# Performance work log

Measured on AMD Instinct MI355X. Metric: run time of the kernel, lower is better.

Reference implementation:

```python
import jax, jax.numpy as jnp
import numpy as np

B, L, DM = 4, 2048, 1024  # batch, seq len (== l_max, global kernel), d_model; head_dim = 1


def setup_inputs() -> dict:
    key = jax.random.key(0)
    ks = jax.random.split(key, 13)
    n = lambda k, shape, s=1.0: jax.random.normal(k, shape, dtype=jnp.float32) * s
    W_SCALE = 0.02   # keeps activations well-conditioned through the chained convs
    K_SCALE = 0.02
    return {
        "u": n(ks[0], (B, L, DM)),
        "Wq": n(ks[1], (DM, DM), W_SCALE), "bq": n(ks[2], (DM,), W_SCALE),
        "Wk": n(ks[3], (DM, DM), W_SCALE), "bk": n(ks[4], (DM,), W_SCALE),
        "Wv": n(ks[5], (DM, DM), W_SCALE), "bv": n(ks[6], (DM,), W_SCALE),
        "k_kernel": n(ks[7], (DM, L), K_SCALE),
        "k_D": n(ks[8], (DM,)),
        "ssm_kernel": n(ks[9], (DM, L), K_SCALE),
        "D": n(ks[10], (DM,)),
        "Wo": n(ks[11], (DM, DM), W_SCALE), "bo": n(ks[12], (DM,), W_SCALE),
    }


def reference(u, Wq, bq, Wk, bk, Wv, bv, k_kernel, k_D, ssm_kernel, D, Wo, bo):
    # u: (B, L, H) with H = d_model (head_dim = 1)
    Lseq = u.shape[1]
    fft_size = 2 * Lseq  # zero-pad to 2L for linear (causal) convolution

    # q/k/v projections -> (B, H, L)
    q = jnp.einsum('blh,dh->bdl', u, Wq) + bq[None, :, None]
    k = jnp.einsum('blh,dh->bdl', u, Wk) + bk[None, :, None]
    v = jnp.einsum('blh,dh->bdl', u, Wv) + bv[None, :, None]

    # shift conv on k: k <- k_kernel * k (causal FFT conv) + k_D * k
    k_kernel_f = jnp.fft.rfft(k_kernel, n=fft_size)           # (H, F)
    k_f = jnp.fft.rfft(k, n=fft_size)                          # (B, H, F)
    shift_k = jnp.fft.irfft(k_kernel_f[None] * k_f, n=fft_size)[..., :Lseq]
    k = shift_k + k_D[None, :, None] * k

    # head_dim == 1: kv outer product collapses to elementwise gate
    kv = k * v                                                 # (B, H, L)

    # ssm conv on kv (torch's 1/fft_size + norm='forward' irfft == standard irfft)
    kv_f = jnp.fft.rfft(kv, n=fft_size)                        # (B, H, F)
    ssm_kernel_f = jnp.fft.rfft(ssm_kernel, n=fft_size)        # (H, F)
    y = jnp.fft.irfft(kv_f * ssm_kernel_f[None], n=fft_size)[..., :Lseq]
    y = y + kv * D[None, :, None]                              # D skip

    # q gating, then output projection
    y = y * q                                                  # (B, H, L)
    y = jnp.swapaxes(y, 1, 2)                                  # (B, L, H)
    return jnp.einsum('blh,oh->blo', y, Wo) + bo
```

## Files before the change

### kernel.cpp

```cpp
#include <hip/hip_runtime.h>
#include <hip/hip_bf16.h>
#include <stdint.h>

#define DM   1024
#define LSEQ 2048
#define NB   4

typedef __attribute__((ext_vector_type(8))) short  short8;
typedef __attribute__((ext_vector_type(4))) float  floatx4;

__device__ __forceinline__ ushort f2b(float x) {
    union { float f; uint32_t u; } v; v.f = x;
    uint32_t b = v.u + 0x7FFF + ((v.u >> 16) & 1);
    return (ushort)(b >> 16);
}
__device__ __forceinline__ float b2f(ushort x) {
    union { uint32_t u; float f; } v; v.u = ((uint32_t)x) << 16;
    return v.f;
}

__global__ __launch_bounds__(256) void cvt_bf16_kernel(const float* __restrict__ in,
                                                       ushort* __restrict__ out, int n8) {
    int i = blockIdx.x * 256 + threadIdx.x;
    if (i >= n8) return;
    const float4* p = (const float4*)in + (size_t)i * 2;
    float4 a = p[0], b = p[1];
    union { ushort us[8]; uint4 v; } o;
    o.us[0] = f2b(a.x); o.us[1] = f2b(a.y); o.us[2] = f2b(a.z); o.us[3] = f2b(a.w);
    o.us[4] = f2b(b.x); o.us[5] = f2b(b.y); o.us[6] = f2b(b.z); o.us[7] = f2b(b.w);
    ((uint4*)out)[i] = o.v;
}

__global__ __launch_bounds__(256) void cvt_w_kernel(const float* __restrict__ Wq,
                                                    const float* __restrict__ Wk,
                                                    const float* __restrict__ Wv,
                                                    const float* __restrict__ Wo,
                                                    ushort* __restrict__ dst) {
    const int per = DM * DM / 8;
    int i = blockIdx.x * 256 + threadIdx.x;
    int r = i / per;
    const float* src = (r == 0) ? Wq : (r == 1) ? Wk : (r == 2) ? Wv : Wo;
    int j = i - r * per;
    const float4* p = (const float4*)src + (size_t)j * 2;
    float4 a = p[0], b = p[1];
    union { ushort us[8]; uint4 v; } o;
    o.us[0] = f2b(a.x); o.us[1] = f2b(a.y); o.us[2] = f2b(a.z); o.us[3] = f2b(a.w);
    o.us[4] = f2b(b.x); o.us[5] = f2b(b.y); o.us[6] = f2b(b.z); o.us[7] = f2b(b.w);
    ((uint4*)dst)[i] = o.v;
}

template <int MODE>
__global__ __launch_bounds__(512, 2) void gemm_8p(const ushort* __restrict__ Aw,
                                                  const ushort* __restrict__ Bw,
                                                  const float* __restrict__ b0,
                                                  const float* __restrict__ b1,
                                                  const float* __restrict__ b2,
                                                  void* __restrict__ C0v,
                                                  void* __restrict__ C1v,
                                                  void* __restrict__ C2v,
                                                  int N, int nbx) {
    constexpr int K = 1024, BK = 64, NT = K / BK;
    __shared__ char lds[131072];

    const int tid   = threadIdx.x;
    const int wave  = tid >> 6;
    const int lane  = tid & 63;
    const int qlane = lane & 15;
    const int qk    = lane >> 4;
    const int z7    = qlane & 7;
    const int wm    = wave >> 2;
    const int wn    = wave & 3;

    int flat = blockIdx.y * nbx + blockIdx.x;
    int nwg  = nbx * gridDim.y;
    int swz  = (flat & 7) * (nwg >> 3) + (flat >> 3);
    const int tn = (swz % nbx) * 256;
    const int tm = (swz / nbx) * 256;

    const int srcChunkOff   = (((lane & 7) ^ (lane >> 3)) * 8);
    const int srcRowInSlice = (lane >> 3);

#define STAGE_H(TT, ISB, H)                                                                   \
    {                                                                                         \
        const ushort* gbase = (ISB) ? Bw : Aw;                                                \
        const int trow = ((ISB) ? tn : tm) + (H) * 128 + wave * 16 + srcRowInSlice;           \
        char* dst = lds + ((ISB) ? 65536 : 0) + ((((TT) & 1) * 2 + (H)) * 16384) + wave * 2048; \
        const int k0_ = (TT) * BK;                                                            \
        _Pragma("unroll")                                                                     \
        for (int j = 0; j < 2; ++j) {                                                         \
            const ushort* src = gbase + (size_t)(trow + j * 8) * K + k0_ + srcChunkOff;       \
            __builtin_amdgcn_global_load_lds(                                                 \
                (const __attribute__((address_space(1))) void*)src,                           \
                (__attribute__((address_space(3))) void*)(dst + j * 1024), 16, 0, 0);         \
        }                                                                                     \
    }

    short8 af[4][2], bf0[2][2], bf1[2][2];
    floatx4 acc[2][2][4][2] = {};

#define LDA(TT, MH)                                                                           \
    {                                                                                         \
        const char* Ab = lds + ((((TT) & 1) * 2 + (MH)) * 16384);                             \
        _Pragma("unroll")                                                                     \
        for (int i = 0; i < 4; ++i) {                                                         \
            int lr = wm * 64 + i * 16 + qlane;                                                \
            _Pragma("unroll")                                                                 \
            for (int ks = 0; ks < 2; ++ks)                                                    \
                af[i][ks] = *(const short8*)(Ab + lr * 128 + (((ks * 4 + qk) ^ z7) << 4));    \
        }                                                                                     \
    }
#define LDB(TT, NH, BF)                                                                       \
    {                                                                                         \
        const char* Bb = lds + 65536 + ((((TT) & 1) * 2 + (NH)) * 16384);                     \
        _Pragma("unroll")                                                                     \
        for (int j = 0; j < 2; ++j) {                                                         \
            int lr = wn * 32 + j * 16 + qlane;                                                \
            _Pragma("unroll")                                                                 \
            for (int ks = 0; ks < 2; ++ks)                                                    \
                BF[j][ks] = *(const short8*)(Bb + lr * 128 + (((ks * 4 + qk) ^ z7) << 4));    \
        }                                                                                     \
    }
#define MFMAQ(MH, NH, BF)                                                                     \
    __builtin_amdgcn_s_setprio(1);                                                           \
    _Pragma("unroll")                                                                         \
    for (int ks = 0; ks < 2; ++ks)                                                            \
        _Pragma("unroll")                                                                     \
        for (int i = 0; i < 4; ++i)                                                           \
            _Pragma("unroll")                                                                 \
            for (int j = 0; j < 2; ++j)                                                       \
                acc[MH][NH][i][j] = __builtin_amdgcn_mfma_f32_16x16x32_bf16(                  \
                    af[i][ks], BF[j][ks], acc[MH][NH][i][j], 0, 0, 0);                        \
    __builtin_amdgcn_s_setprio(0);
#define BAR  __builtin_amdgcn_s_barrier(); __builtin_amdgcn_sched_barrier(0)
#define LGKM0 asm volatile("s_waitcnt lgkmcnt(0)" ::: "memory"); __builtin_amdgcn_sched_barrier(0)

    STAGE_H(0, 0, 0); STAGE_H(0, 1, 0); STAGE_H(0, 1, 1); STAGE_H(0, 0, 1);
    STAGE_H(1, 0, 0); STAGE_H(1, 1, 0); STAGE_H(1, 1, 1);
    asm volatile("s_waitcnt vmcnt(6)" ::: "memory");
    __builtin_amdgcn_s_barrier();
    __builtin_amdgcn_sched_barrier(0);

    for (int t = 0; t < NT; ++t) {
        LDA(t, 0);
        LDB(t, 0, bf0);
        if (t + 1 < NT) STAGE_H(t + 1, 0, 1);
        BAR; LGKM0;
        MFMAQ(0, 0, bf0);
        BAR;
        LDB(t, 1, bf1);
        if (t + 2 < NT) STAGE_H(t + 2, 0, 0);
        BAR; LGKM0;
        MFMAQ(0, 1, bf1);
        BAR;
        LDA(t, 1);
        if (t + 2 < NT) STAGE_H(t + 2, 1, 0);
        BAR; LGKM0;
        MFMAQ(1, 0, bf0);
        BAR;
        if (t + 2 < NT) STAGE_H(t + 2, 1, 1);
        if (t + 2 < NT)      { asm volatile("s_waitcnt vmcnt(6)" ::: "memory"); }
        else if (t + 1 < NT) { asm volatile("s_waitcnt vmcnt(0)" ::: "memory"); }
        BAR; LGKM0;
        MFMAQ(1, 1, bf1);
        BAR;
    }
#undef STAGE_H
#undef LDA
#undef LDB
#undef MFMAQ
#undef BAR
#undef LGKM0

#pragma unroll
    for (int mh = 0; mh < 2; ++mh)
#pragma unroll
    for (int nh = 0; nh < 2; ++nh)
#pragma unroll
    for (int i = 0; i < 4; ++i)
#pragma unroll
    for (int j = 0; j < 2; ++j) {
        int n  = tn + nh * 128 + wn * 32 + j * 16 + qlane;
        int m0 = tm + mh * 128 + wm * 64 + i * 16 + qk * 4;
        if (MODE == 0) {
            int proj = n >> 10, dd = n & (DM - 1);
            const float* bb = (proj == 0) ? b0 : (proj == 1) ? b1 : b2;
            ushort* Cb      = (ushort*)((proj == 0) ? C0v : (proj == 1) ? C1v : C2v);
            float bv = bb[dd];
            int b = m0 >> 11, l = m0 & (LSEQ - 1);
            ushort4 val;
            val.x = f2b(acc[mh][nh][i][j][0] + bv);
            val.y = f2b(acc[mh][nh][i][j][1] + bv);
            val.z = f2b(acc[mh][nh][i][j][2] + bv);
            val.w = f2b(acc[mh][nh][i][j][3] + bv);
            *(ushort4*)(Cb + ((size_t)b * DM + dd) * LSEQ + l) = val;
        } else {
            float* C0 = (float*)C0v;
            float bv = b0[n];
#pragma unroll
            for (int r = 0; r < 4; ++r)
                C0[(size_t)(m0 + r) * N + n] = acc[mh][nh][i][j][r] + bv;
        }
    }
}

template <int MODE>
__global__ __launch_bounds__(512, 2) void gemm_bt2(const ushort* __restrict__ Aw,
                                                   const ushort* __restrict__ Bw,
                                                   const float* __restrict__ b0,
                                                   const float* __restrict__ b1,
                                                   const float* __restrict__ b2,
                                                   void* __restrict__ C0v,
                                                   void* __restrict__ C1v,
                                                   void* __restrict__ C2v,
                                                   int M, int N, int K, int nbx) {
    constexpr int BM = 128, BN = 256, BK = 64;
    constexpr int BUFB = 49152;
    __shared__ char lds[3 * BUFB];

    const int tid   = threadIdx.x;
    const int wave  = tid >> 6;
    const int lane  = tid & 63;
    const int qlane = lane & 15;
    const int qk    = lane >> 4;

    int flat = blockIdx.y * nbx + blockIdx.x;
    int nwg  = nbx * gridDim.y;
    int swz  = (flat & 7) * (nwg >> 3) + (flat >> 3);
    const int tn = (swz % nbx) * BN;
    const int tm = (swz / nbx) * BM;

    const int wmo = (wave >> 2) * 64;
    const int wno = (wave & 3) * 64;
    const int NT  = K / BK;

#define STAGE(kt, p)                                                                          \
    {                                                                                         \
        const int k0_ = (kt) * BK;                                                            \
        char* Ab_ = lds + (p) * BUFB;                                                         \
        char* Bb_ = Ab_ + 16384;                                                              \
        _Pragma("unroll")                                                                     \
        for (int j = 0; j < 2; ++j) {                                                         \
            int id = wave * 64 + lane + j * 512;                                              \
            int row = id >> 3, s = id & 7;                                                    \
            const ushort* src = Aw + (size_t)(tm + row) * K + k0_ + ((s ^ (row & 7)) * 8);    \
            __builtin_amdgcn_global_load_lds((const __attribute__((address_space(1))) void*)src, \
                (__attribute__((address_space(3))) void*)(Ab_ + wave * 1024 + j * 8192), 16, 0, 0); \
        }                                                                                     \
        _Pragma("unroll")                                                                     \
        for (int j = 0; j < 4; ++j) {                                                         \
            int id = wave * 64 + lane + j * 512;                                              \
            int row = id >> 3, s = id & 7;                                                    \
            const ushort* src = Bw + (size_t)(tn + row) * K + k0_ + ((s ^ (row & 7)) * 8);    \
            __builtin_amdgcn_global_load_lds((const __attribute__((address_space(1))) void*)src, \
                (__attribute__((address_space(3))) void*)(Bb_ + wave * 1024 + j * 8192), 16, 0, 0); \
        }                                                                                     \
    }

    floatx4 acc[4][4] = {};

    STAGE(0, 0);
    STAGE(1, 1);

    const int z7 = qlane & 7;

    for (int t = 0; t < NT; ++t) {
        const int cur = t % 3;
        if (t < NT - 1) asm volatile("s_waitcnt vmcnt(6)" ::: "memory");
        else            asm volatile("s_waitcnt vmcnt(0)" ::: "memory");
        __builtin_amdgcn_s_barrier();
        __builtin_amdgcn_sched_barrier(0);

        if (t + 2 < NT) STAGE(t + 2, (t + 2) % 3);

        const char* Ab = lds + cur * BUFB;
        const char* Bb = Ab + 16384;
#pragma unroll
        for (int kk = 0; kk < 2; ++kk) {
            const int slot = ((kk * 4 + qk) ^ z7) << 4;
            short8 af[4], bfv[4];
#pragma unroll
            for (int i = 0; i < 4; ++i) {
                int r = wmo + i * 16 + qlane;
                af[i] = *(const short8*)(Ab + r * 128 + slot);
            }
#pragma unroll
            for (int j = 0; j < 4; ++j) {
                int r = wno + j * 16 + qlane;
                bfv[j] = *(const short8*)(Bb + r * 128 + slot);
            }
            __builtin_amdgcn_s_setprio(1);
#pragma unroll
            for (int i = 0; i < 4; ++i)
#pragma unroll
                for (int j = 0; j < 4; ++j)
                    acc[i][j] = __builtin_amdgcn_mfma_f32_16x16x32_bf16(af[i], bfv[j], acc[i][j], 0, 0, 0);
            __builtin_amdgcn_s_setprio(0);
        }
    }
#undef STAGE

#pragma unroll
    for (int i = 0; i < 4; ++i) {
#pragma unroll
        for (int j = 0; j < 4; ++j) {
            int n  = tn + wno + j * 16 + qlane;
            int m0 = tm + wmo + i * 16 + qk * 4;
            if (MODE == 0) {
                int proj = n >> 10, dd = n & (DM - 1);
                const float* bb = (proj == 0) ? b0 : (proj == 1) ? b1 : b2;
                ushort* Cb      = (ushort*)((proj == 0) ? C0v : (proj == 1) ? C1v : C2v);
                float bv = bb[dd];
                int b = m0 >> 11, l = m0 & (LSEQ - 1);
                ushort4 val;
                val.x = f2b(acc[i][j][0] + bv);
                val.y = f2b(acc[i][j][1] + bv);
                val.z = f2b(acc[i][j][2] + bv);
                val.w = f2b(acc[i][j][3] + bv);
                *(ushort4*)(Cb + ((size_t)b * DM + dd) * LSEQ + l) = val;
            } else {
                float* C0 = (float*)C0v;
                float bv = b0[n];
#pragma unroll
                for (int r = 0; r < 4; ++r)
                    C0[(size_t)(m0 + r) * N + n] = acc[i][j][r] + bv;
            }
        }
    }
}

#define KSTR 2096
#define XSTR 2248

__global__ __launch_bounds__(512) void conv_mfma_kernel(const ushort* __restrict__ x,
                                                        const float* __restrict__ ker,
                                                        const float* __restrict__ scale,
                                                        const ushort* __restrict__ gate,
                                                        ushort* __restrict__ out) {
    __shared__ ushort krev[KSTR];
    __shared__ ushort xs[4 * XSTR];
    const int d    = blockIdx.x;
    const int tid  = threadIdx.x;
    const int wave = tid >> 6;
    const int lane = tid & 63;

    {
        int b = wave >> 1, half = wave & 1;
        const ushort* src = x + ((size_t)b * DM + d) * LSEQ + half * 1024 + lane * 8;
        char* dst = (char*)xs + b * (XSTR * 2) + 256 + half * 2048;
#pragma unroll
        for (int c = 0; c < 2; ++c)
            __builtin_amdgcn_global_load_lds((const __attribute__((address_space(1))) void*)(src + c * 512),
                                             (__attribute__((address_space(3))) void*)(dst + c * 1024),
                                             16, 0, 0);
    }
    {
        const float* krow = ker + (size_t)d * LSEQ;
        int e0 = tid * 4;
        float4 kv = *(const float4*)(krow + e0);
        ushort4 o;
        o.x = f2b(kv.w); o.y = f2b(kv.z); o.z = f2b(kv.y); o.w = f2b(kv.x);
        *(ushort4*)(krev + (2060 - e0)) = o;
        uint4 z = {0, 0, 0, 0};
        if (tid < 2)  *(uint4*)((char*)krev + tid * 16) = z;
        if (tid >= 2 && tid < 6) *(uint4*)((char*)krev + 4128 + (tid - 2) * 16) = z;
        if (tid >= 64 && tid < 128) {
            int b = (tid - 64) >> 4, c = (tid - 64) & 15;
            *(uint4*)((char*)xs + b * (XSTR * 2) + c * 16) = z;
        }
        if (tid >= 128 && tid < 144) {
            int b = (tid - 128) >> 2, c = (tid - 128) & 3;
            *(uint4*)((char*)xs + b * (XSTR * 2) + 4352 + c * 16) = z;
        }
    }
    __syncthreads();

    const int qn = lane & 15;
    const int qk = lane >> 4;

    int g[2] = {wave, 15 - wave};
    const int smax_all = 128 * (15 - wave) + 128;

    const int lbase = (qn & 3) * XSTR + 128 + 16 * (qn >> 2) + 8 * qk;

    floatx4 acc[2][2] = {};

    short8 fE[2], fO[2];
#pragma unroll
    for (int gi = 0; gi < 2; ++gi) {
        fE[gi] = *(const short8*)(xs + lbase + 128 * g[gi] + 64);
        fO[gi] = *(const short8*)(xs + lbase + 128 * g[gi] + 32);
    }

#define CSTEP(SS, FP)                                                                        \
    {                                                                                        \
        int b_el = 2063 - qn + 8 * qk - (SS);                                                \
        int A0 = b_el & ~3;                                                                  \
        uint2 w0 = *(const uint2*)(krev + A0);                                               \
        uint2 w1 = *(const uint2*)(krev + A0 + 4);                                           \
        uint2 w2 = *(const uint2*)(krev + A0 + 8);                                           \
        int qsel = (b_el >> 1) & 1;                                                          \
        uint sh  = (uint)(b_el & 1) * 16u;                                                   \
        uint e0 = qsel ? w0.y : w0.x;                                                        \
        uint e1 = qsel ? w1.x : w0.y;                                                        \
        uint e2 = qsel ? w1.y : w1.x;                                                        \
        uint e3 = qsel ? w2.x : w1.y;                                                        \
        uint e4 = qsel ? w2.y : w2.x;                                                        \
        union { uint u[4]; short8 v; } Af;                                                   \
        Af.u[0] = __builtin_amdgcn_alignbit(e1, e0, sh);                                     \
        Af.u[1] = __builtin_amdgcn_alignbit(e2, e1, sh);                                     \
        Af.u[2] = __builtin_amdgcn_alignbit(e3, e2, sh);                                     \
        Af.u[3] = __builtin_amdgcn_alignbit(e4, e3, sh);                                     \
        _Pragma("unroll")                                                                    \
        for (int gi = 0; gi < 2; ++gi) {                                                     \
            if ((SS) <= 128 * g[gi] + 128) {                                                 \
                short8 fN = *(const short8*)(xs + lbase + 128 * g[gi] - (SS));               \
                acc[gi][0] = __builtin_amdgcn_mfma_f32_16x16x32_bf16(Af.v, fN, acc[gi][0], 0, 0, 0); \
                acc[gi][1] = __builtin_amdgcn_mfma_f32_16x16x32_bf16(Af.v, FP[gi], acc[gi][1], 0, 0, 0); \
                FP[gi] = fN;                                                                 \
            }                                                                                \
        }                                                                                    \
    }

    for (int s = 0; s <= smax_all; s += 64) {
        CSTEP(s, fE);
        if (s + 32 <= smax_all) CSTEP(s + 32, fO);
    }
#undef CSTEP

    const float sc = scale[d];
#pragma unroll
    for (int gi = 0; gi < 2; ++gi) {
#pragma unroll
        for (int m = 0; m < 2; ++m) {
            int p  = 8 * g[gi] + 4 * m + (qn >> 2);
            int b  = qn & 3;
            int l0 = 16 * p + 4 * qk;
            size_t off = ((size_t)b * DM + d) * LSEQ + l0;
            ushort4 xv = *(const ushort4*)(xs + b * XSTR + 128 + l0);
            ushort4 gv = *(const ushort4*)(gate + off);
            ushort4 ov;
            ov.x = f2b((acc[gi][m][0] + sc * b2f(xv.x)) * b2f(gv.x));
            ov.y = f2b((acc[gi][m][1] + sc * b2f(xv.y)) * b2f(gv.y));
            ov.z = f2b((acc[gi][m][2] + sc * b2f(xv.z)) * b2f(gv.z));
            ov.w = f2b((acc[gi][m][3] + sc * b2f(xv.w)) * b2f(gv.w));
            *(ushort4*)(out + off) = ov;
        }
    }
}

__global__ __launch_bounds__(256) void transpose_bf16(const ushort* __restrict__ in,
                                                      ushort* __restrict__ out) {
    __shared__ ushort t[32][36];
    const int l0 = blockIdx.x * 32;
    const int d0 = blockIdx.y * 32;
    const int b  = blockIdx.z;
    const int q  = threadIdx.x & 7;
    const int r  = threadIdx.x >> 3;
    *(ushort4*)(&t[r][q * 4]) = *(const ushort4*)(in + ((size_t)b * DM + d0 + r) * LSEQ + l0 + q * 4);
    __syncthreads();
    ushort4 o;
    o.x = t[q * 4 + 0][r]; o.y = t[q * 4 + 1][r]; o.z = t[q * 4 + 2][r]; o.w = t[q * 4 + 3][r];
    *(ushort4*)(out + ((size_t)b * LSEQ + l0 + r) * DM + d0 + q * 4) = o;
}

extern "C" void kernel_launch(void* const* d_in, const int* in_sizes, int n_in,
                              void* d_out, int out_size, void* d_ws, size_t ws_size,
                              hipStream_t stream) {
    const float* u        = (const float*)d_in[0];
    const float* Wq       = (const float*)d_in[1];
    const float* bq       = (const float*)d_in[2];
    const float* Wk       = (const float*)d_in[3];
    const float* bk       = (const float*)d_in[4];
    const float* Wv       = (const float*)d_in[5];
    const float* bv       = (const float*)d_in[6];
    const float* k_kernel = (const float*)d_in[7];
    const float* k_D      = (const float*)d_in[8];
    const float* ssm_ker  = (const float*)d_in[9];
    const float* Dv       = (const float*)d_in[10];
    const float* Wo       = (const float*)d_in[11];
    const float* bo       = (const float*)d_in[12];
    float* outp = (float*)d_out;

    char* ws = (char*)d_ws;
    ushort* Q    = (ushort*)(ws);
    ushort* KV   = (ushort*)(ws + (16ull << 20));
    ushort* V    = (ushort*)(ws + (32ull << 20));
    ushort* U16  = (ushort*)(ws + (48ull << 20));
    ushort* YT   = (ushort*)(ws + (64ull << 20));
    ushort* Wcat = (ushort*)(ws + (80ull << 20));

    cvt_bf16_kernel<<<(NB * LSEQ * DM / 8) / 256, 256, 0, stream>>>(u, U16, NB * LSEQ * DM / 8);
    cvt_w_kernel<<<(4 * DM * DM / 8) / 256, 256, 0, stream>>>(Wq, Wk, Wv, Wo, Wcat);

    dim3 g1(3 * DM / 256, NB * LSEQ / 256);
    gemm_8p<0><<<g1, 512, 0, stream>>>(U16, Wcat, bq, bk, bv, Q, KV, V,
                                       3 * DM, 3 * DM / 256);

    conv_mfma_kernel<<<DM, 512, 0, stream>>>(KV, k_kernel, k_D, V, KV);
    conv_mfma_kernel<<<DM, 512, 0, stream>>>(KV, ssm_ker, Dv, Q, KV);

    dim3 g2(LSEQ / 32, DM / 32, NB);
    transpose_bf16<<<g2, 256, 0, stream>>>(KV, YT);

    dim3 g3(DM / 256, NB * LSEQ / 128);
    gemm_bt2<1><<<g3, 512, 0, stream>>>(YT, Wcat + 3 * DM * DM, bo, bo, bo,
                                        outp, outp, outp, NB * LSEQ, DM, DM, DM / 256);
}
```

Measured before the change: 173.2 us.

## Software-pipeline LDS fragment loads across MFMA quadrants and fuse conversion kernels

New measurement: 166.4 us. -4.0%, faster.

```diff
diff --git a/kernel.cpp b/kernel.cpp
--- a/kernel.cpp
+++ b/kernel.cpp
@@ -19,34 +19,31 @@
     return v.f;
 }
 
-__global__ __launch_bounds__(256) void cvt_bf16_kernel(const float* __restrict__ in,
-                                                       ushort* __restrict__ out, int n8) {
-    int i = blockIdx.x * 256 + threadIdx.x;
-    if (i >= n8) return;
-    const float4* p = (const float4*)in + (size_t)i * 2;
-    float4 a = p[0], b = p[1];
-    union { ushort us[8]; uint4 v; } o;
-    o.us[0] = f2b(a.x); o.us[1] = f2b(a.y); o.us[2] = f2b(a.z); o.us[3] = f2b(a.w);
-    o.us[4] = f2b(b.x); o.us[5] = f2b(b.y); o.us[6] = f2b(b.z); o.us[7] = f2b(b.w);
-    ((uint4*)out)[i] = o.v;
-}
-
-__global__ __launch_bounds__(256) void cvt_w_kernel(const float* __restrict__ Wq,
-                                                    const float* __restrict__ Wk,
-                                                    const float* __restrict__ Wv,
-                                                    const float* __restrict__ Wo,
-                                                    ushort* __restrict__ dst) {
+__global__ __launch_bounds__(256) void cvt_all_kernel(const float* __restrict__ u,
+                                                      const float* __restrict__ Wq,
+                                                      const float* __restrict__ Wk,
+                                                      const float* __restrict__ Wv,
+                                                      const float* __restrict__ Wo,
+                                                      ushort* __restrict__ U16,
+                                                      ushort* __restrict__ Wcat) {
+    const int nu  = NB * LSEQ * DM / 8;
     const int per = DM * DM / 8;
     int i = blockIdx.x * 256 + threadIdx.x;
-    int r = i / per;
-    const float* src = (r == 0) ? Wq : (r == 1) ? Wk : (r == 2) ? Wv : Wo;
-    int j = i - r * per;
+    const float* src; ushort* dst; int j;
+    if (i < nu) { src = u; dst = U16; j = i; }
+    else {
+        int k = i - nu;
+        int r = k / per;
+        src = (r == 0) ? Wq : (r == 1) ? Wk : (r == 2) ? Wv : Wo;
+        dst = Wcat + (size_t)r * (DM * DM);
+        j = k - r * per;
+    }
     const float4* p = (const float4*)src + (size_t)j * 2;
     float4 a = p[0], b = p[1];
     union { ushort us[8]; uint4 v; } o;
     o.us[0] = f2b(a.x); o.us[1] = f2b(a.y); o.us[2] = f2b(a.z); o.us[3] = f2b(a.w);
     o.us[4] = f2b(b.x); o.us[5] = f2b(b.y); o.us[6] = f2b(b.z); o.us[7] = f2b(b.w);
-    ((uint4*)dst)[i] = o.v;
+    *(uint4*)(dst + (size_t)j * 8) = o.v;
 }
 
 template <int MODE>
@@ -95,10 +92,10 @@
         }                                                                                     \
     }
 
-    short8 af[4][2], bf0[2][2], bf1[2][2];
+    short8 af[4][2], af2[4][2], bf0[2][2], bf1[2][2];
     floatx4 acc[2][2][4][2] = {};
 
-#define LDA(TT, MH)                                                                           \
+#define LDA(TT, MH, AF)                                                                       \
     {                                                                                         \
         const char* Ab = lds + ((((TT) & 1) * 2 + (MH)) * 16384);                             \
         _Pragma("unroll")                                                                     \
@@ -106,7 +103,7 @@
             int lr = wm * 64 + i * 16 + qlane;                                                \
             _Pragma("unroll")                                                                 \
             for (int ks = 0; ks < 2; ++ks)                                                    \
-                af[i][ks] = *(const short8*)(Ab + lr * 128 + (((ks * 4 + qk) ^ z7) << 4));    \
+                AF[i][ks] = *(const short8*)(Ab + lr * 128 + (((ks * 4 + qk) ^ z7) << 4));    \
         }                                                                                     \
     }
 #define LDB(TT, NH, BF)                                                                       \
@@ -120,7 +117,7 @@
                 BF[j][ks] = *(const short8*)(Bb + lr * 128 + (((ks * 4 + qk) ^ z7) << 4));    \
         }                                                                                     \
     }
-#define MFMAQ(MH, NH, BF)                                                                     \
+#define MFMAQ(MH, NH, AF, BF)                                                                 \
     __builtin_amdgcn_s_setprio(1);                                                           \
     _Pragma("unroll")                                                                         \
     for (int ks = 0; ks < 2; ++ks)                                                            \
@@ -129,47 +126,40 @@
             _Pragma("unroll")                                                                 \
             for (int j = 0; j < 2; ++j)                                                       \
                 acc[MH][NH][i][j] = __builtin_amdgcn_mfma_f32_16x16x32_bf16(                  \
-                    af[i][ks], BF[j][ks], acc[MH][NH][i][j], 0, 0, 0);                        \
+                    AF[i][ks], BF[j][ks], acc[MH][NH][i][j], 0, 0, 0);                        \
     __builtin_amdgcn_s_setprio(0);
-#define BAR  __builtin_amdgcn_s_barrier(); __builtin_amdgcn_sched_barrier(0)
-#define LGKM0 asm volatile("s_waitcnt lgkmcnt(0)" ::: "memory"); __builtin_amdgcn_sched_barrier(0)
+#define BARX  __builtin_amdgcn_s_barrier(); __builtin_amdgcn_sched_barrier(0)
 
     STAGE_H(0, 0, 0); STAGE_H(0, 1, 0); STAGE_H(0, 1, 1); STAGE_H(0, 0, 1);
     STAGE_H(1, 0, 0); STAGE_H(1, 1, 0); STAGE_H(1, 1, 1);
     asm volatile("s_waitcnt vmcnt(6)" ::: "memory");
-    __builtin_amdgcn_s_barrier();
-    __builtin_amdgcn_sched_barrier(0);
+    BARX;
+    LDA(0, 0, af); LDB(0, 0, bf0);
 
     for (int t = 0; t < NT; ++t) {
-        LDA(t, 0);
-        LDB(t, 0, bf0);
         if (t + 1 < NT) STAGE_H(t + 1, 0, 1);
-        BAR; LGKM0;
-        MFMAQ(0, 0, bf0);
-        BAR;
         LDB(t, 1, bf1);
+        MFMAQ(0, 0, af, bf0);
+        BARX;
         if (t + 2 < NT) STAGE_H(t + 2, 0, 0);
-        BAR; LGKM0;
-        MFMAQ(0, 1, bf1);
-        BAR;
-        LDA(t, 1);
+        LDA(t, 1, af2);
+        MFMAQ(0, 1, af, bf1);
+        BARX;
         if (t + 2 < NT) STAGE_H(t + 2, 1, 0);
-        BAR; LGKM0;
-        MFMAQ(1, 0, bf0);
-        BAR;
+        MFMAQ(1, 0, af2, bf0);
+        BARX;
         if (t + 2 < NT) STAGE_H(t + 2, 1, 1);
         if (t + 2 < NT)      { asm volatile("s_waitcnt vmcnt(6)" ::: "memory"); }
         else if (t + 1 < NT) { asm volatile("s_waitcnt vmcnt(0)" ::: "memory"); }
-        BAR; LGKM0;
-        MFMAQ(1, 1, bf1);
-        BAR;
+        BARX;
+        if (t + 1 < NT) { LDA(t + 1, 0, af); LDB(t + 1, 0, bf0); }
+        MFMAQ(1, 1, af2, bf1);
     }
 #undef STAGE_H
 #undef LDA
 #undef LDB
 #undef MFMAQ
-#undef BAR
-#undef LGKM0
+#undef BARX
 
 #pragma unroll
     for (int mh = 0; mh < 2; ++mh)
@@ -489,8 +479,8 @@
     ushort* YT   = (ushort*)(ws + (64ull << 20));
     ushort* Wcat = (ushort*)(ws + (80ull << 20));
 
-    cvt_bf16_kernel<<<(NB * LSEQ * DM / 8) / 256, 256, 0, stream>>>(u, U16, NB * LSEQ * DM / 8);
-    cvt_w_kernel<<<(4 * DM * DM / 8) / 256, 256, 0, stream>>>(Wq, Wk, Wv, Wo, Wcat);
+    const int nu = NB * LSEQ * DM / 8, nw = 4 * DM * DM / 8;
+    cvt_all_kernel<<<(nu + nw) / 256, 256, 0, stream>>>(u, Wq, Wk, Wv, Wo, U16, Wcat);
 
     dim3 g1(3 * DM / 256, NB * LSEQ / 256);
     gemm_8p<0><<<g1, 512, 0, stream>>>(U16, Wcat, bq, bk, bv, Q, KV, V,
```
